# Kernel optimization log

Hardware: AMD Instinct MI355X
Metric: run time of the kernel (lower is better)

The kernel has to match this reference:

```python
import jax, jax.numpy as jnp
import numpy as np

B, C, H, W = 4, 128, 64, 64


def setup_inputs() -> dict:
    key = jax.random.key(0)
    k1, k2 = jax.random.split(key)
    x = jax.random.normal(k1, (B, C, H, W), dtype=jnp.float32)
    # 1x1 conv kv_mapper: weight [C_out, C_in], bias [C_out]; C_out == C_in == C
    W_kv = jax.random.normal(k2, (C, C), dtype=jnp.float32) * (1.0 / np.sqrt(C))
    b_kv = jnp.zeros((C,), dtype=jnp.float32)
    return {"x": x, "W_kv": W_kv, "b_kv": b_kv}


def reference(x, W_kv, b_kv):
    b, c, h, w = x.shape
    # kv_mapper: 1x1 conv  -> v: [b, c, h, w]
    v = jnp.einsum('bchw,oc->bohw', x, W_kv) + b_kv[None, :, None, None]
    # rearrange 'b c h w -> b (h w) c'
    L = h * w
    values = v.reshape(b, c, L).transpose(0, 2, 1)    # keys == values
    queries = x.reshape(b, c, L).transpose(0, 2, 1)
    # scaled dot-product attention, full [b, L, L] scores
    scores = jnp.einsum('blc,btc->blt', queries, values) / jnp.sqrt(jnp.asarray(c, x.dtype))
    attn = jax.nn.softmax(scores, axis=-1)
    out = jnp.einsum('blt,btv->blv', attn, values)    # [b, L, c]
    # rearrange 'b (h w) c -> b c h w'
    return out.transpose(0, 2, 1).reshape(b, c, h, w)
```

## Files before the change

### kernel.cpp

```cpp
#include <hip/hip_runtime.h>

#define LQ 4096
#define CH 128
#define NB 4
#define QSCALE 0.12753139626233174f
#define ASTR 136
#define BSTR 72
#define MAXCH 8

#if defined(__has_builtin)
#if __has_builtin(__builtin_amdgcn_mfma_f32_16x16x16bf16_1k)
#define HAVE_MFMA16 1
#endif
#endif

typedef __attribute__((ext_vector_type(8))) unsigned short ushort8;
typedef __attribute__((ext_vector_type(4))) unsigned short ushort4v;
typedef __attribute__((ext_vector_type(4))) short short4v;
typedef __attribute__((ext_vector_type(8))) __bf16 bf16x8;
typedef __attribute__((ext_vector_type(4))) float f32x4;

__device__ inline unsigned short f2bf(float f) {
    unsigned int u = __builtin_bit_cast(unsigned int, f);
    u += 0x7fffu + ((u >> 16) & 1u);
    return (unsigned short)(u >> 16);
}
__device__ inline float bf2f(unsigned short h) {
    unsigned int u = (unsigned int)h << 16;
    return __builtin_bit_cast(float, u);
}
__device__ inline unsigned int bfpack2(float a, float b) {
    unsigned int ua = __builtin_bit_cast(unsigned int, a) + 0x8000u;
    unsigned int ub = __builtin_bit_cast(unsigned int, b) + 0x8000u;
    return (ua >> 16) | (ub & 0xffff0000u);
}

__global__ __launch_bounds__(256) void prep_kernel(
    const float* __restrict__ x, const float* __restrict__ Wkv,
    const float* __restrict__ bkv,
    unsigned short* __restrict__ Vt, unsigned short* __restrict__ Vc)
{
    __shared__ __align__(16) unsigned short xs[64 * 136];
    __shared__ __align__(16) unsigned short vs[128 * 72];
    const int tid = threadIdx.x;
    const int lane = tid & 63;
    const int wave = tid >> 6;
    const int quad = lane >> 4, l16 = lane & 15;
    const int b = blockIdx.x & 3;
    const int l0 = (blockIdx.x >> 2) << 6;

    {
        const f32x4* xg4 = (const f32x4*)(x + (size_t)b * CH * LQ + l0);
        #pragma unroll
        for (int i = 0; i < 8; ++i) {
            int idx = i * 256 + tid;
            int c = idx >> 4, l4 = idx & 15;
            f32x4 v = xg4[c * (LQ / 4) + l4];
            #pragma unroll
            for (int m = 0; m < 4; ++m) xs[(l4 * 4 + m) * 136 + c] = f2bf(v[m]);
        }
    }
    __syncthreads();

    const int wo = wave * 32;
    f32x4 acc[2][4];
    #pragma unroll
    for (int ot = 0; ot < 2; ++ot)
        #pragma unroll
        for (int lt = 0; lt < 4; ++lt) acc[ot][lt] = f32x4{0.f, 0.f, 0.f, 0.f};

    #pragma unroll
    for (int kc = 0; kc < 4; ++kc) {
        bf16x8 af[2];
        #pragma unroll
        for (int ot = 0; ot < 2; ++ot) {
            const float* wrow = Wkv + (size_t)(wo + ot * 16 + l16) * CH + kc * 32 + quad * 8;
            ushort8 a;
            #pragma unroll
            for (int j = 0; j < 8; ++j) a[j] = f2bf(wrow[j]);
            af[ot] = __builtin_bit_cast(bf16x8, a);
        }
        #pragma unroll
        for (int lt = 0; lt < 4; ++lt) {
            bf16x8 bf = __builtin_bit_cast(bf16x8,
                *(const ushort8*)(xs + (lt * 16 + l16) * 136 + kc * 32 + quad * 8));
            #pragma unroll
            for (int ot = 0; ot < 2; ++ot)
                acc[ot][lt] = __builtin_amdgcn_mfma_f32_16x16x32_bf16(af[ot], bf, acc[ot][lt], 0, 0, 0);
        }
    }
    #pragma unroll
    for (int ot = 0; ot < 2; ++ot) {
        float bias[4];
        #pragma unroll
        for (int r = 0; r < 4; ++r) bias[r] = bkv[wo + ot * 16 + quad * 4 + r];
        #pragma unroll
        for (int lt = 0; lt < 4; ++lt)
            #pragma unroll
            for (int r = 0; r < 4; ++r)
                vs[(wo + ot * 16 + quad * 4 + r) * 72 + lt * 16 + l16] =
                    f2bf(acc[ot][lt][r] + bias[r]);
    }
    __syncthreads();
    #pragma unroll
    for (int i = 0; i < 4; ++i) {
        const int chunk = i * 256 + tid;
        const int o = chunk >> 3, l8 = chunk & 7;
        *(ushort8*)(Vc + ((size_t)b * CH + o) * LQ + l0 + l8 * 8) =
            *(const ushort8*)(vs + o * 72 + l8 * 8);
    }
    #pragma unroll
    for (int i = 0; i < 4; ++i) {
        const int chunk = i * 256 + tid;
        const int l = chunk >> 4, og = chunk & 15;
        ushort8 v;
        #pragma unroll
        for (int k = 0; k < 8; ++k) v[k] = vs[(og * 8 + k) * 72 + l];
        *(ushort8*)(Vt + ((size_t)b * LQ + l0 + l) * CH + og * 8) = v;
    }
}

__global__ __launch_bounds__(256, 2) void attn_kernel(
    const float* __restrict__ x, const unsigned short* __restrict__ Vt,
    const unsigned short* __restrict__ Vc,
    unsigned short* __restrict__ Opart, float* __restrict__ Lsum, int titers)
{
    __shared__ __align__(16) unsigned short tileA[64 * ASTR];
    __shared__ __align__(16) unsigned short tileB[128 * BSTR];
    const int tid = threadIdx.x;
    const int wave = tid >> 6, lane = tid & 63;
    const int quad = lane >> 4, l16 = lane & 15;
    const int b = blockIdx.x & 3;
    const int rest = blockIdx.x >> 2;
    const int qtile = rest & 31;
    const int chunk = rest >> 5;
    const int q0w = (qtile << 7) + (wave << 5);
    const int tbase = chunk * titers * 64;

    const unsigned short* vtb = Vt + (size_t)b * LQ * CH;
    const unsigned short* vcb = Vc + (size_t)b * CH * LQ;

    bf16x8 qf[2][4];
    #pragma unroll
    for (int mt = 0; mt < 2; ++mt)
        #pragma unroll
        for (int kc = 0; kc < 4; ++kc) {
            ushort8 v;
            #pragma unroll
            for (int j = 0; j < 8; ++j) {
                int c = kc * 32 + quad * 8 + j;
                v[j] = f2bf(x[((size_t)b * CH + c) * LQ + q0w + mt * 16 + l16] * QSCALE);
            }
            qf[mt][kc] = __builtin_bit_cast(bf16x8, v);
        }

    f32x4 oacc[2][8];
    #pragma unroll
    for (int mt = 0; mt < 2; ++mt)
        #pragma unroll
        for (int i = 0; i < 8; ++i) oacc[mt][i] = f32x4{0.f, 0.f, 0.f, 0.f};
    float lsum[2] = {0.f, 0.f};

    ushort8 RA[4], RB[4];
    {
        const int t0 = tbase;
        #pragma unroll
        for (int i = 0; i < 4; ++i) {
            const int ci = i * 256 + tid;
            RA[i] = *(const ushort8*)(vtb + (size_t)(t0 + (ci >> 4)) * CH + (ci & 15) * 8);
        }
        #pragma unroll
        for (int i = 0; i < 4; ++i) {
            const int ci = i * 256 + tid;
            RB[i] = *(const ushort8*)(vcb + (size_t)(ci >> 3) * LQ + t0 + (ci & 7) * 8);
        }
    }

    for (int it = 0; it < titers; ++it) {
        __syncthreads();
        #pragma unroll
        for (int i = 0; i < 4; ++i) {
            const int ci = i * 256 + tid;
            *(ushort8*)(tileA + (ci >> 4) * ASTR + (ci & 15) * 8) = RA[i];
        }
        #pragma unroll
        for (int i = 0; i < 4; ++i) {
            const int ci = i * 256 + tid;
            *(ushort8*)(tileB + (ci >> 3) * BSTR + (ci & 7) * 8) = RB[i];
        }
        __syncthreads();
        {
            const int t0n = (it + 1 < titers) ? tbase + (it + 1) * 64 : tbase;
            #pragma unroll
            for (int i = 0; i < 4; ++i) {
                const int ci = i * 256 + tid;
                RA[i] = *(const ushort8*)(vtb + (size_t)(t0n + (ci >> 4)) * CH + (ci & 15) * 8);
            }
            #pragma unroll
            for (int i = 0; i < 4; ++i) {
                const int ci = i * 256 + tid;
                RB[i] = *(const ushort8*)(vcb + (size_t)(ci >> 3) * LQ + t0n + (ci & 7) * 8);
            }
        }
        #pragma unroll
        for (int nt = 0; nt < 4; ++nt) {
            bf16x8 vA[4];
            #pragma unroll
            for (int kc = 0; kc < 4; ++kc)
                vA[kc] = __builtin_bit_cast(bf16x8,
                    *(const ushort8*)(tileA + (nt * 16 + l16) * ASTR + kc * 32 + quad * 8));
            f32x4 s[2];
            #pragma unroll
            for (int mt = 0; mt < 2; ++mt) {
                s[mt] = f32x4{0.f, 0.f, 0.f, 0.f};
                #pragma unroll
                for (int kc = 0; kc < 4; ++kc)
                    s[mt] = __builtin_amdgcn_mfma_f32_16x16x32_bf16(vA[kc], qf[mt][kc], s[mt], 0, 0, 0);
            }
#ifdef HAVE_MFMA16
            short4v pf[2];
#else
            bf16x8 pf[2];
#endif
            #pragma unroll
            for (int mt = 0; mt < 2; ++mt) {
                float p0 = __builtin_amdgcn_exp2f(s[mt][0]);
                float p1 = __builtin_amdgcn_exp2f(s[mt][1]);
                float p2 = __builtin_amdgcn_exp2f(s[mt][2]);
                float p3 = __builtin_amdgcn_exp2f(s[mt][3]);
                lsum[mt] += (p0 + p1) + (p2 + p3);
                unsigned int lo = bfpack2(p0, p1);
                unsigned int hi = bfpack2(p2, p3);
#ifdef HAVE_MFMA16
                ushort4v pk;
                pk[0] = (unsigned short)lo; pk[1] = (unsigned short)(lo >> 16);
                pk[2] = (unsigned short)hi; pk[3] = (unsigned short)(hi >> 16);
                pf[mt] = __builtin_bit_cast(short4v, pk);
#else
                ushort8 pk;
                pk[0] = (unsigned short)lo; pk[1] = (unsigned short)(lo >> 16);
                pk[2] = (unsigned short)hi; pk[3] = (unsigned short)(hi >> 16);
                pk[4] = 0; pk[5] = 0; pk[6] = 0; pk[7] = 0;
                pf[mt] = __builtin_bit_cast(bf16x8, pk);
#endif
            }
            #pragma unroll
            for (int nc = 0; nc < 8; ++nc) {
                ushort4v d = *(const ushort4v*)(tileB +
                    (nc * 16 + l16) * BSTR + nt * 16 + quad * 4);
#ifdef HAVE_MFMA16
                short4v vB = __builtin_bit_cast(short4v, d);
                #pragma unroll
                for (int mt = 0; mt < 2; ++mt)
                    oacc[mt][nc] = __builtin_amdgcn_mfma_f32_16x16x16bf16_1k(
                        pf[mt], vB, oacc[mt][nc], 0, 0, 0);
#else
                ushort8 vb;
                vb[0] = d[0]; vb[1] = d[1]; vb[2] = d[2]; vb[3] = d[3];
                vb[4] = 0; vb[5] = 0; vb[6] = 0; vb[7] = 0;
                bf16x8 vB = __builtin_bit_cast(bf16x8, vb);
                #pragma unroll
                for (int mt = 0; mt < 2; ++mt)
                    oacc[mt][nc] = __builtin_amdgcn_mfma_f32_16x16x32_bf16(
                        pf[mt], vB, oacc[mt][nc], 0, 0, 0);
#endif
            }
        }
    }
    const size_t pbase = ((size_t)(chunk * NB + b) * LQ);
    #pragma unroll
    for (int mt = 0; mt < 2; ++mt) {
        float v = lsum[mt];
        v += __shfl_xor(v, 16);
        v += __shfl_xor(v, 32);
        if (lane < 16) Lsum[pbase + q0w + mt * 16 + lane] = v;
    }
    #pragma unroll
    for (int mt = 0; mt < 2; ++mt)
        #pragma unroll
        for (int r = 0; r < 4; ++r) {
            const int q = q0w + mt * 16 + quad * 4 + r;
            unsigned short* orow = Opart + (pbase + q) * CH + l16;
            #pragma unroll
            for (int nc = 0; nc < 8; ++nc) orow[nc * 16] = f2bf(oacc[mt][nc][r]);
        }
}

__global__ __launch_bounds__(256) void combine_kernel(
    const unsigned short* __restrict__ Opart, const float* __restrict__ Lsum,
    float* __restrict__ out, int nchunk)
{
    __shared__ __align__(16) float ls[32 * 132];
    __shared__ float linv[32];
    const int tid = threadIdx.x;
    const int b = blockIdx.x & 3;
    const int q0 = (blockIdx.x >> 2) << 5;

    if (tid < 32) {
        float s = 0.f;
        for (int ch = 0; ch < nchunk; ++ch) s += Lsum[(size_t)(ch * NB + b) * LQ + q0 + tid];
        linv[tid] = 1.0f / s;
    }
    __syncthreads();
    {
        const int c8 = (tid & 15) * 8, qg = tid >> 4;
        #pragma unroll
        for (int i = 0; i < 2; ++i) {
            const int q = qg * 2 + i;
            float s[8];
            #pragma unroll
            for (int k = 0; k < 8; ++k) s[k] = 0.f;
            for (int ch = 0; ch < nchunk; ++ch) {
                ushort8 p = *(const ushort8*)(Opart +
                    ((size_t)(ch * NB + b) * LQ + q0 + q) * CH + c8);
                #pragma unroll
                for (int k = 0; k < 8; ++k) s[k] += bf2f(p[k]);
            }
            const float li = linv[q];
            f32x4 o0, o1;
            #pragma unroll
            for (int k = 0; k < 4; ++k) { o0[k] = s[k] * li; o1[k] = s[k + 4] * li; }
            *(f32x4*)(ls + q * 132 + c8) = o0;
            *(f32x4*)(ls + q * 132 + c8 + 4) = o1;
        }
    }
    __syncthreads();
    {
        const int c = tid & 127, qh = tid >> 7;
        float* dst = out + ((size_t)b * CH + c) * LQ + q0 + qh * 16;
        #pragma unroll
        for (int i = 0; i < 4; ++i) {
            f32x4 o;
            #pragma unroll
            for (int r = 0; r < 4; ++r) o[r] = ls[(qh * 16 + i * 4 + r) * 132 + c];
            ((f32x4*)dst)[i] = o;
        }
    }
}

extern "C" void kernel_launch(void* const* d_in, const int* in_sizes, int n_in,
                              void* d_out, int out_size, void* d_ws, size_t ws_size,
                              hipStream_t stream) {
    const float* x   = (const float*)d_in[0];
    const float* Wkv = (const float*)d_in[1];
    const float* bkv = (const float*)d_in[2];
    float* out = (float*)d_out;

    const size_t vElems = (size_t)NB * LQ * CH;
    unsigned short* Vt = (unsigned short*)d_ws;
    unsigned short* Vc = Vt + vElems;
    float* Lsum = (float*)(Vc + vElems);
    unsigned short* Opart = (unsigned short*)(Lsum + (size_t)MAXCH * NB * LQ);

    int nchunk = MAXCH;
    const size_t fixed = 2 * vElems * 2 + (size_t)MAXCH * NB * LQ * 4;
    while (nchunk > 1 && fixed + (size_t)nchunk * NB * LQ * CH * 2 > ws_size) nchunk >>= 1;
    const int titers = (LQ / 64) / nchunk;

    prep_kernel<<<dim3(256), dim3(256), 0, stream>>>(x, Wkv, bkv, Vt, Vc);
    attn_kernel<<<dim3(128 * nchunk), dim3(256), 0, stream>>>(x, Vt, Vc, Opart, Lsum, titers);
    combine_kernel<<<dim3(512), dim3(256), 0, stream>>>(Opart, Lsum, out, nchunk);
}
```

Baseline: 131.4 us.

## Pre-tile V into MFMA fragment layout and double-buffer via direct global-to-LDS loads

The prep kernel now writes both V copies as per-64-key tiles already arranged in the lane order the MFMA fragments need. The attention kernel fetches those tiles with global_load_lds straight into a double-buffered LDS ring, which removes the register staging, one of the two barriers per iteration and the strided LDS reads. Each wave also now handles 64 queries instead of 32, so every loaded K/V tile is reused across twice as many queries and the grid is halved. The cost is more accumulator and query registers per wave, which risks spills or lower occupancy, and fewer blocks to spread across the CUs.

Measured after the change: 250.2 us. 90.5% more time.

```diff
diff --git a/kernel.cpp b/kernel.cpp
--- a/kernel.cpp
+++ b/kernel.cpp
@@ -4,9 +4,8 @@
 #define CH 128
 #define NB 4
 #define QSCALE 0.12753139626233174f
-#define ASTR 136
-#define BSTR 72
 #define MAXCH 8
+#define TILE_HW 8192
 
 #if defined(__has_builtin)
 #if __has_builtin(__builtin_amdgcn_mfma_f32_16x16x16bf16_1k)
@@ -34,11 +33,16 @@
     unsigned int ub = __builtin_bit_cast(unsigned int, b) + 0x8000u;
     return (ua >> 16) | (ub & 0xffff0000u);
 }
+__device__ inline void gload_lds16(const unsigned short* g, unsigned short* l) {
+    __builtin_amdgcn_global_load_lds(
+        (const __attribute__((address_space(1))) unsigned int*)(g),
+        (__attribute__((address_space(3))) unsigned int*)(l), 16, 0, 0);
+}
 
 __global__ __launch_bounds__(256) void prep_kernel(
     const float* __restrict__ x, const float* __restrict__ Wkv,
     const float* __restrict__ bkv,
-    unsigned short* __restrict__ Vt, unsigned short* __restrict__ Vc)
+    unsigned short* __restrict__ Vt2, unsigned short* __restrict__ Vc2)
 {
     __shared__ __align__(16) unsigned short xs[64 * 136];
     __shared__ __align__(16) unsigned short vs[128 * 72];
@@ -47,7 +51,8 @@
     const int wave = tid >> 6;
     const int quad = lane >> 4, l16 = lane & 15;
     const int b = blockIdx.x & 3;
-    const int l0 = (blockIdx.x >> 2) << 6;
+    const int T = blockIdx.x >> 2;
+    const int l0 = T << 6;
 
     {
         const f32x4* xg4 = (const f32x4*)(x + (size_t)b * CH * LQ + l0);
@@ -102,47 +107,54 @@
                     f2bf(acc[ot][lt][r] + bias[r]);
     }
     __syncthreads();
+    const size_t tbase = ((size_t)b * 64 + T) * TILE_HW;
     #pragma unroll
     for (int i = 0; i < 4; ++i) {
-        const int chunk = i * 256 + tid;
-        const int o = chunk >> 3, l8 = chunk & 7;
-        *(ushort8*)(Vc + ((size_t)b * CH + o) * LQ + l0 + l8 * 8) =
-            *(const ushort8*)(vs + o * 72 + l8 * 8);
+        const int ci = i * 256 + tid;
+        const int g = ci >> 6, ls = ci & 63;
+        const int nt = g >> 2, kc = g & 3, qs = ls >> 4, l16s = ls & 15;
+        ushort8 v;
+        #pragma unroll
+        for (int j = 0; j < 8; ++j) v[j] = vs[(kc * 32 + qs * 8 + j) * 72 + nt * 16 + l16s];
+        *(ushort8*)(Vt2 + tbase + (size_t)ci * 8) = v;
     }
     #pragma unroll
     for (int i = 0; i < 4; ++i) {
-        const int chunk = i * 256 + tid;
-        const int l = chunk >> 4, og = chunk & 15;
+        const int ci = i * 256 + tid;
+        const int g = ci >> 6, ls = ci & 63;
+        const int nt = g >> 2, p = g & 3, qs = ls >> 4, l16s = ls & 15;
+        ushort4v a = *(const ushort4v*)(vs + (p * 32 + l16s) * 72 + nt * 16 + qs * 4);
+        ushort4v c2 = *(const ushort4v*)(vs + (p * 32 + 16 + l16s) * 72 + nt * 16 + qs * 4);
         ushort8 v;
         #pragma unroll
-        for (int k = 0; k < 8; ++k) v[k] = vs[(og * 8 + k) * 72 + l];
-        *(ushort8*)(Vt + ((size_t)b * LQ + l0 + l) * CH + og * 8) = v;
+        for (int j = 0; j < 4; ++j) { v[j] = a[j]; v[j + 4] = c2[j]; }
+        *(ushort8*)(Vc2 + tbase + (size_t)ci * 8) = v;
     }
 }
 
 __global__ __launch_bounds__(256, 2) void attn_kernel(
-    const float* __restrict__ x, const unsigned short* __restrict__ Vt,
-    const unsigned short* __restrict__ Vc,
+    const float* __restrict__ x, const unsigned short* __restrict__ Vt2,
+    const unsigned short* __restrict__ Vc2,
     unsigned short* __restrict__ Opart, float* __restrict__ Lsum, int titers)
 {
-    __shared__ __align__(16) unsigned short tileA[64 * ASTR];
-    __shared__ __align__(16) unsigned short tileB[128 * BSTR];
+    __shared__ __align__(16) unsigned short bufA[2][TILE_HW];
+    __shared__ __align__(16) unsigned short bufB[2][TILE_HW];
     const int tid = threadIdx.x;
     const int wave = tid >> 6, lane = tid & 63;
     const int quad = lane >> 4, l16 = lane & 15;
     const int b = blockIdx.x & 3;
     const int rest = blockIdx.x >> 2;
-    const int qtile = rest & 31;
-    const int chunk = rest >> 5;
-    const int q0w = (qtile << 7) + (wave << 5);
-    const int tbase = chunk * titers * 64;
-
-    const unsigned short* vtb = Vt + (size_t)b * LQ * CH;
-    const unsigned short* vcb = Vc + (size_t)b * CH * LQ;
-
-    bf16x8 qf[2][4];
-    #pragma unroll
-    for (int mt = 0; mt < 2; ++mt)
+    const int qtile = rest & 15;
+    const int chunk = rest >> 4;
+    const int q0w = (qtile << 8) + (wave << 6);
+    const int Tbase = chunk * titers;
+
+    const unsigned short* vtb = Vt2 + (size_t)b * 64 * TILE_HW;
+    const unsigned short* vcb = Vc2 + (size_t)b * 64 * TILE_HW;
+
+    bf16x8 qf[4][4];
+    #pragma unroll
+    for (int mt = 0; mt < 4; ++mt)
         #pragma unroll
         for (int kc = 0; kc < 4; ++kc) {
             ushort8 v;
@@ -154,76 +166,52 @@
             qf[mt][kc] = __builtin_bit_cast(bf16x8, v);
         }
 
-    f32x4 oacc[2][8];
-    #pragma unroll
-    for (int mt = 0; mt < 2; ++mt)
+    f32x4 oacc[4][8];
+    #pragma unroll
+    for (int mt = 0; mt < 4; ++mt)
         #pragma unroll
         for (int i = 0; i < 8; ++i) oacc[mt][i] = f32x4{0.f, 0.f, 0.f, 0.f};
-    float lsum[2] = {0.f, 0.f};
-
-    ushort8 RA[4], RB[4];
-    {
-        const int t0 = tbase;
-        #pragma unroll
-        for (int i = 0; i < 4; ++i) {
-            const int ci = i * 256 + tid;
-            RA[i] = *(const ushort8*)(vtb + (size_t)(t0 + (ci >> 4)) * CH + (ci & 15) * 8);
-        }
-        #pragma unroll
-        for (int i = 0; i < 4; ++i) {
-            const int ci = i * 256 + tid;
-            RB[i] = *(const ushort8*)(vcb + (size_t)(ci >> 3) * LQ + t0 + (ci & 7) * 8);
-        }
-    }
+    float lsum[4] = {0.f, 0.f, 0.f, 0.f};
+
+    auto issue = [&](int T, int nb) {
+        const unsigned short* sa = vtb + (size_t)T * TILE_HW + lane * 8;
+        const unsigned short* sb = vcb + (size_t)T * TILE_HW + lane * 8;
+        #pragma unroll
+        for (int g = 0; g < 4; ++g) {
+            const int go = (wave * 4 + g) * 512;
+            gload_lds16(sa + go, &bufA[nb][go]);
+            gload_lds16(sb + go, &bufB[nb][go]);
+        }
+    };
+    issue(Tbase, 0);
 
     for (int it = 0; it < titers; ++it) {
         __syncthreads();
-        #pragma unroll
-        for (int i = 0; i < 4; ++i) {
-            const int ci = i * 256 + tid;
-            *(ushort8*)(tileA + (ci >> 4) * ASTR + (ci & 15) * 8) = RA[i];
-        }
-        #pragma unroll
-        for (int i = 0; i < 4; ++i) {
-            const int ci = i * 256 + tid;
-            *(ushort8*)(tileB + (ci >> 3) * BSTR + (ci & 7) * 8) = RB[i];
-        }
-        __syncthreads();
-        {
-            const int t0n = (it + 1 < titers) ? tbase + (it + 1) * 64 : tbase;
-            #pragma unroll
-            for (int i = 0; i < 4; ++i) {
-                const int ci = i * 256 + tid;
-                RA[i] = *(const ushort8*)(vtb + (size_t)(t0n + (ci >> 4)) * CH + (ci & 15) * 8);
-            }
-            #pragma unroll
-            for (int i = 0; i < 4; ++i) {
-                const int ci = i * 256 + tid;
-                RB[i] = *(const ushort8*)(vcb + (size_t)(ci >> 3) * LQ + t0n + (ci & 7) * 8);
-            }
-        }
+        if (it + 1 < titers) issue(Tbase + it + 1, (it + 1) & 1);
+        const unsigned short* A = bufA[it & 1];
+        const unsigned short* B = bufB[it & 1];
         #pragma unroll
         for (int nt = 0; nt < 4; ++nt) {
             bf16x8 vA[4];
             #pragma unroll
             for (int kc = 0; kc < 4; ++kc)
                 vA[kc] = __builtin_bit_cast(bf16x8,
-                    *(const ushort8*)(tileA + (nt * 16 + l16) * ASTR + kc * 32 + quad * 8));
-            f32x4 s[2];
-            #pragma unroll
-            for (int mt = 0; mt < 2; ++mt) {
+                    *(const ushort8*)(A + (nt * 4 + kc) * 512 + lane * 8));
+            f32x4 s[4];
+            #pragma unroll
+            for (int mt = 0; mt < 4; ++mt) {
                 s[mt] = f32x4{0.f, 0.f, 0.f, 0.f};
                 #pragma unroll
                 for (int kc = 0; kc < 4; ++kc)
                     s[mt] = __builtin_amdgcn_mfma_f32_16x16x32_bf16(vA[kc], qf[mt][kc], s[mt], 0, 0, 0);
             }
 #ifdef HAVE_MFMA16
-            short4v pf[2];
+            short4v pf[4];
 #else
-            bf16x8 pf[2];
-#endif
-            #pragma unroll
-            for (int mt = 0; mt < 2; ++mt) {
+            bf16x8 pf[4];
+#endif
+            #pragma unroll
+            for (int mt = 0; mt < 4; ++mt) {
                 float p0 = __builtin_amdgcn_exp2f(s[mt][0]);
                 float p1 = __builtin_amdgcn_exp2f(s[mt][1]);
                 float p2 = __builtin_amdgcn_exp2f(s[mt][2]);
@@ -245,38 +233,43 @@
 #endif
             }
             #pragma unroll
-            for (int nc = 0; nc < 8; ++nc) {
-                ushort4v d = *(const ushort4v*)(tileB +
-                    (nc * 16 + l16) * BSTR + nt * 16 + quad * 4);
+            for (int p = 0; p < 4; ++p) {
+                ushort8 d8 = *(const ushort8*)(B + (nt * 4 + p) * 512 + lane * 8);
+                #pragma unroll
+                for (int h = 0; h < 2; ++h) {
+                    ushort4v f;
+                    #pragma unroll
+                    for (int j = 0; j < 4; ++j) f[j] = d8[h * 4 + j];
 #ifdef HAVE_MFMA16
-                short4v vB = __builtin_bit_cast(short4v, d);
-                #pragma unroll
-                for (int mt = 0; mt < 2; ++mt)
-                    oacc[mt][nc] = __builtin_amdgcn_mfma_f32_16x16x16bf16_1k(
-                        pf[mt], vB, oacc[mt][nc], 0, 0, 0);
+                    short4v vB = __builtin_bit_cast(short4v, f);
+                    #pragma unroll
+                    for (int mt = 0; mt < 4; ++mt)
+                        oacc[mt][p * 2 + h] = __builtin_amdgcn_mfma_f32_16x16x16bf16_1k(
+                            pf[mt], vB, oacc[mt][p * 2 + h], 0, 0, 0);
 #else
-                ushort8 vb;
-                vb[0] = d[0]; vb[1] = d[1]; vb[2] = d[2]; vb[3] = d[3];
-                vb[4] = 0; vb[5] = 0; vb[6] = 0; vb[7] = 0;
-                bf16x8 vB = __builtin_bit_cast(bf16x8, vb);
-                #pragma unroll
-                for (int mt = 0; mt < 2; ++mt)
-                    oacc[mt][nc] = __builtin_amdgcn_mfma_f32_16x16x32_bf16(
-                        pf[mt], vB, oacc[mt][nc], 0, 0, 0);
-#endif
+                    ushort8 vb;
+                    #pragma unroll
+                    for (int j = 0; j < 4; ++j) { vb[j] = f[j]; vb[j + 4] = 0; }
+                    bf16x8 vB = __builtin_bit_cast(bf16x8, vb);
+                    #pragma unroll
+                    for (int mt = 0; mt < 4; ++mt)
+                        oacc[mt][p * 2 + h] = __builtin_amdgcn_mfma_f32_16x16x32_bf16(
+                            pf[mt], vB, oacc[mt][p * 2 + h], 0, 0, 0);
+#endif
+                }
             }
         }
     }
     const size_t pbase = ((size_t)(chunk * NB + b) * LQ);
     #pragma unroll
-    for (int mt = 0; mt < 2; ++mt) {
+    for (int mt = 0; mt < 4; ++mt) {
         float v = lsum[mt];
         v += __shfl_xor(v, 16);
         v += __shfl_xor(v, 32);
         if (lane < 16) Lsum[pbase + q0w + mt * 16 + lane] = v;
     }
     #pragma unroll
-    for (int mt = 0; mt < 2; ++mt)
+    for (int mt = 0; mt < 4; ++mt)
         #pragma unroll
         for (int r = 0; r < 4; ++r) {
             const int q = q0w + mt * 16 + quad * 4 + r;
@@ -347,9 +340,9 @@
     float* out = (float*)d_out;
 
     const size_t vElems = (size_t)NB * LQ * CH;
-    unsigned short* Vt = (unsigned short*)d_ws;
-    unsigned short* Vc = Vt + vElems;
-    float* Lsum = (float*)(Vc + vElems);
+    unsigned short* Vt2 = (unsigned short*)d_ws;
+    unsigned short* Vc2 = Vt2 + vElems;
+    float* Lsum = (float*)(Vc2 + vElems);
     unsigned short* Opart = (unsigned short*)(Lsum + (size_t)MAXCH * NB * LQ);
 
     int nchunk = MAXCH;
@@ -357,7 +350,7 @@
     while (nchunk > 1 && fixed + (size_t)nchunk * NB * LQ * CH * 2 > ws_size) nchunk >>= 1;
     const int titers = (LQ / 64) / nchunk;
 
-    prep_kernel<<<dim3(256), dim3(256), 0, stream>>>(x, Wkv, bkv, Vt, Vc);
-    attn_kernel<<<dim3(128 * nchunk), dim3(256), 0, stream>>>(x, Vt, Vc, Opart, Lsum, titers);
+    prep_kernel<<<dim3(256), dim3(256), 0, stream>>>(x, Wkv, bkv, Vt2, Vc2);
+    attn_kernel<<<dim3(64 * nchunk), dim3(256), 0, stream>>>(x, Vt2, Vc2, Opart, Lsum, titers);
     combine_kernel<<<dim3(512), dim3(256), 0, stream>>>(Opart, Lsum, out, nchunk);
 }
```
